# Performance work log

Hardware: AMD Instinct MI355X
Metric: run time of the kernel (lower is better)

The kernel has to match this reference:

```python
import jax, jax.numpy as jnp
import numpy as np

NUM_FRAMES = 6
HEADS = 16
DIM_HEAD = 64


def setup_inputs() -> dict:
    key = jax.random.key(0)
    ks = jax.random.split(key, 7)
    D = 1024
    x = jax.random.normal(ks[0], (12, 1024, D), dtype=jnp.float32)
    context = jax.random.normal(ks[1], (2, 1024, D), dtype=jnp.float32)
    s = 1.0 / np.sqrt(D)
    Wq = jax.random.normal(ks[2], (D, D), dtype=jnp.float32) * s
    Wk = jax.random.normal(ks[3], (D, D), dtype=jnp.float32) * s
    Wv = jax.random.normal(ks[4], (D, D), dtype=jnp.float32) * s
    Wo = jax.random.normal(ks[5], (D, D), dtype=jnp.float32) * s
    bo = jnp.zeros((D,), dtype=jnp.float32)
    return {"x": x, "context": context, "Wq": Wq, "Wk": Wk, "Wv": Wv, "Wo": Wo, "bo": bo}


def reference(x, context, Wq, Wk, Wv, Wo, bo):
    B, S, D = x.shape  # B=12, S=1024, D=1024
    scale = DIM_HEAD ** (-0.5)
    ab = B // NUM_FRAMES  # actual batch after frame inflation
    xr = x.reshape(ab, NUM_FRAMES * S, D)  # [ab, 6144, D]
    # Linear projections (torch Linear: y = x @ W.T)
    q = xr @ Wq.T            # [ab, Sq, inner]
    k = context @ Wk.T       # [ab, Sk, inner]
    v = context @ Wv.T
    Sq = q.shape[1]
    Sk = k.shape[1]
    q = q.reshape(ab, Sq, HEADS, DIM_HEAD).transpose(0, 2, 1, 3)  # [ab,h,Sq,d]
    k = k.reshape(ab, Sk, HEADS, DIM_HEAD).transpose(0, 2, 1, 3)
    v = v.reshape(ab, Sk, HEADS, DIM_HEAD).transpose(0, 2, 1, 3)
    attn = jnp.einsum("bhqd,bhkd->bhqk", q, k) * scale
    attn = jax.nn.softmax(attn, axis=-1)
    out = jnp.einsum("bhqk,bhkd->bhqd", attn, v)
    out = out.transpose(0, 2, 1, 3).reshape(ab, Sq, HEADS * DIM_HEAD)
    out = out @ Wo.T + bo  # dropout is identity at p=0 / eval
    return out.reshape(B, S, D)
```

## Files before the change

kernel.cpp:

```cpp
#include <hip/hip_runtime.h>

typedef short bf16x8 __attribute__((ext_vector_type(8)));
typedef float floatx4 __attribute__((ext_vector_type(4)));
typedef unsigned short u16;
typedef unsigned int u32;

__device__ __forceinline__ u16 f2bf(float f) {
  u32 u = __float_as_uint(f);
  u += 0x7FFF + ((u >> 16) & 1);
  return (u16)(u >> 16);
}
__device__ __forceinline__ u32 packbf(float a, float b) {
  return (u32)f2bf(a) | ((u32)f2bf(b) << 16);
}
__device__ __forceinline__ u32 permpack(u32 a_bits, u32 b_bits) {
  return __builtin_amdgcn_perm(b_bits, a_bits, 0x07060302u);
}

__device__ __forceinline__ float ex2(float x) {
#if __has_builtin(__builtin_amdgcn_exp2f)
  return __builtin_amdgcn_exp2f(x);
#else
  float r;
  asm("v_exp_f32 %0, %1" : "=v"(r) : "v"(x));
  return r;
#endif
}

__device__ __forceinline__ void gload_lds16(const u16* g, u16* l) {
  __builtin_amdgcn_global_load_lds(
      (const __attribute__((address_space(1))) void*)(const void*)g,
      (__attribute__((address_space(3))) void*)(void*)l, 16, 0, 0);
}

__device__ __forceinline__ void bb_mainloop(const u16* __restrict__ A,
                                            const u16* __restrict__ W,
                                            u16* As, u16* Ws, int m0, int n0,
                                            floatx4 acc[4][4]) {
  const int tid = threadIdx.x, lane = tid & 63, w = tid >> 6;
  const int wm = w & 1, wn = w >> 1;
  const int m16 = lane & 15, quad = lane >> 4;
  const int lr = lane >> 2;
  const int sc = (lane & 3) * 8;

  const u16* Ag = A + (size_t)(m0 + w * 32 + lr) * 1024 + sc;
  const u16* Wg = W + (size_t)(n0 + w * 32 + lr) * 1024 + sc;
  u16* const Asl = &As[(w * 32) * 32];
  u16* const Wsl = &Ws[(w * 32) * 32];

#pragma unroll
  for (int i = 0; i < 4; ++i)
#pragma unroll
    for (int j = 0; j < 4; ++j) acc[i][j] = (floatx4)0.0f;

  for (int kt = 0; kt < 32; ++kt) {
    gload_lds16(Ag, Asl);
    gload_lds16(Ag + 16 * 1024, Asl + 16 * 32);
    gload_lds16(Wg, Wsl);
    gload_lds16(Wg + 16 * 1024, Wsl + 16 * 32);
    Ag += 32;
    Wg += 32;
    __syncthreads();
    bf16x8 af[4], bfr[4];
#pragma unroll
    for (int t = 0; t < 4; ++t) {
      af[t]  = *(const bf16x8*)&As[(wm * 64 + t * 16 + m16) * 32 + quad * 8];
      bfr[t] = *(const bf16x8*)&Ws[(wn * 64 + t * 16 + m16) * 32 + quad * 8];
    }
#pragma unroll
    for (int i = 0; i < 4; ++i)
#pragma unroll
      for (int j = 0; j < 4; ++j)
        acc[i][j] = __builtin_amdgcn_mfma_f32_16x16x32_bf16(af[i], bfr[j],
                                                            acc[i][j], 0, 0, 0);
    __syncthreads();
  }
}

__global__ __launch_bounds__(256) void gemm_qkv(
    const u16* __restrict__ xb, const u16* __restrict__ ctxb,
    const u16* __restrict__ wqb, const u16* __restrict__ wkb,
    const u16* __restrict__ wvb, u16* __restrict__ Qb, u16* __restrict__ Kbuf,
    u16* __restrict__ Vtb) {
  __shared__ u16 As[128 * 32];
  __shared__ u16 Ws[128 * 32];
  const int lane = threadIdx.x & 63, w = threadIdx.x >> 6;
  const int wm = w & 1, wn = w >> 1;
  const int m16 = lane & 15, quad = lane >> 4;
  const int y = blockIdx.y;
  const u16 *A, *W;
  int m0, mode;
  if (y < 96)       { A = xb;   W = wqb; m0 = y * 128;         mode = 0; }
  else if (y < 112) { A = ctxb; W = wkb; m0 = (y - 96) * 128;  mode = 1; }
  else              { A = ctxb; W = wvb; m0 = (y - 112) * 128; mode = 2; }
  const int n0 = blockIdx.x * 128;
  floatx4 acc[4][4];
  bb_mainloop(A, W, As, Ws, m0, n0, acc);
  const float cs = (mode == 0) ? 0.18033688011112042f : 1.0f;
#pragma unroll
  for (int j = 0; j < 4; ++j) {
    const int col = n0 + wn * 64 + j * 16 + m16;
#pragma unroll
    for (int i = 0; i < 4; ++i)
#pragma unroll
      for (int r = 0; r < 4; ++r) {
        const int row = m0 + wm * 64 + i * 16 + quad * 4 + r;
        const u16 v = f2bf(acc[i][j][r] * cs);
        if (mode == 0)
          Qb[(size_t)row * 1024 + col] = v;
        else if (mode == 1)
          Kbuf[(size_t)row * 1024 + col] = v;
        else
          Vtb[((size_t)((row >> 10) * 1024 + col)) * 1024 + (row & 1023)] = v;
      }
  }
}

__global__ __launch_bounds__(256) void gemm_out(const u16* __restrict__ A,
                                                const u16* __restrict__ W,
                                                float* __restrict__ C,
                                                const float* __restrict__ bias) {
  __shared__ u16 As[128 * 32];
  __shared__ u16 Ws[128 * 32];
  const int lane = threadIdx.x & 63, w = threadIdx.x >> 6;
  const int wm = w & 1, wn = w >> 1;
  const int m16 = lane & 15, quad = lane >> 4;
  const int n0 = blockIdx.x * 128, m0 = blockIdx.y * 128;
  floatx4 acc[4][4];
  bb_mainloop(A, W, As, Ws, m0, n0, acc);
#pragma unroll
  for (int j = 0; j < 4; ++j) {
    const int col = n0 + wn * 64 + j * 16 + m16;
    const float bv = bias[col];
#pragma unroll
    for (int i = 0; i < 4; ++i)
#pragma unroll
      for (int r = 0; r < 4; ++r) {
        const int row = m0 + wm * 64 + i * 16 + quad * 4 + r;
        C[(size_t)row * 1024 + col] = acc[i][j][r] + bv;
      }
  }
}

__global__ __launch_bounds__(256) void cvt_all(
    const float* __restrict__ x, const float* __restrict__ ctx,
    const float* __restrict__ wq, const float* __restrict__ wk,
    const float* __restrict__ wv, const float* __restrict__ wo,
    u16* __restrict__ xb, u16* __restrict__ ctxb, u16* __restrict__ wqb,
    u16* __restrict__ wkb, u16* __restrict__ wvb, u16* __restrict__ wob) {
  const u32 i = blockIdx.x * 256 + threadIdx.x;
  const float* s;
  u16* d;
  u32 o;
  if (i < 3145728u)      { s = x;   d = xb;   o = i; }
  else if (i < 3670016u) { s = ctx; d = ctxb; o = i - 3145728u; }
  else if (i < 3932160u) { s = wq;  d = wqb;  o = i - 3670016u; }
  else if (i < 4194304u) { s = wk;  d = wkb;  o = i - 3932160u; }
  else if (i < 4456448u) { s = wv;  d = wvb;  o = i - 4194304u; }
  else                   { s = wo;  d = wob;  o = i - 4456448u; }
  const float4 v = ((const float4*)s)[o];
  uint2 p;
  p.x = packbf(v.x, v.y);
  p.y = packbf(v.z, v.w);
  ((uint2*)d)[o] = p;
}

__global__ __launch_bounds__(256, 4) void attn_flash(
    const u16* __restrict__ Q, const u16* __restrict__ Kb,
    const u16* __restrict__ Vt, u16* __restrict__ O) {
  __shared__ u16 Kl[2 * 64 * 32];
  __shared__ u16 Vl[2 * 64 * 32];
  __shared__ u32 Pl[4 * 32 * 36];
  const int tid = threadIdx.x, lane = tid & 63, w = tid >> 6;
  const int m16 = lane & 15, quad = lane >> 4;
  const int h = blockIdx.y, b = blockIdx.z;
  const int q0 = blockIdx.x * 128 + w * 32;
  u32* const pbase = &Pl[w * 32 * 36];

  bf16x8 aq[2][2];
#pragma unroll
  for (int qt = 0; qt < 2; ++qt)
#pragma unroll
    for (int ks = 0; ks < 2; ++ks)
      aq[qt][ks] =
          *(const bf16x8*)&Q[((size_t)(b * 6144 + q0 + qt * 16 + m16)) * 1024 +
                             h * 64 + ks * 32 + quad * 8];

  const int wk = w & 1, wh = w >> 1;
  const u16* kg = Kb + ((size_t)(b * 1024 + wh * 32 + (lane >> 2))) * 1024 +
                  h * 64 + wk * 32 + (lane & 3) * 8;
  const u16* vg = Vt + ((size_t)(b * 16 + h)) * 65536 +
                  (size_t)(wh * 32 + (lane >> 2)) * 1024 + wk * 32 +
                  (lane & 3) * 8;
  u16* const klb = &Kl[wk * 2048 + wh * 1024];
  u16* const vlb = &Vl[wk * 2048 + wh * 1024];

  bf16x8 vone;
#pragma unroll
  for (int e = 0; e < 8; ++e) vone[e] = (short)0x3F80;

  floatx4 oacc[2][4];
#pragma unroll
  for (int qt = 0; qt < 2; ++qt)
#pragma unroll
    for (int mtd = 0; mtd < 4; ++mtd) oacc[qt][mtd] = (floatx4)0.0f;
  floatx4 lacc[2];
  lacc[0] = (floatx4)0.0f;
  lacc[1] = (floatx4)0.0f;

#pragma unroll 1
  for (int kt = 0; kt < 16; ++kt) {
    gload_lds16(kg, klb);
    gload_lds16(kg + 16 * 1024, klb + 512);
    gload_lds16(vg, vlb);
    gload_lds16(vg + 16 * 1024, vlb + 512);
    kg += 64 * 1024;
    vg += 64;
    __syncthreads();

    floatx4 sst[2][4];
#pragma unroll
    for (int mt = 0; mt < 4; ++mt) {
      const int row = mt * 16 + m16;
      const bf16x8 kf0 = *(const bf16x8*)&Kl[row * 32 + quad * 8];
      const bf16x8 kf1 = *(const bf16x8*)&Kl[2048 + row * 32 + quad * 8];
#pragma unroll
      for (int qt = 0; qt < 2; ++qt) {
        floatx4 t = (floatx4)0.0f;
        t = __builtin_amdgcn_mfma_f32_16x16x32_bf16(kf0, aq[qt][0], t, 0, 0, 0);
        sst[qt][mt] =
            __builtin_amdgcn_mfma_f32_16x16x32_bf16(kf1, aq[qt][1], t, 0, 0, 0);
      }
    }
#pragma unroll
    for (int qt = 0; qt < 2; ++qt) {
      u32* const prow = &pbase[(qt * 16 + m16) * 36 + quad * 2];
#pragma unroll
      for (int mt = 0; mt < 4; ++mt) {
        const u32 b0 = __float_as_uint(ex2(sst[qt][mt][0]));
        const u32 b1 = __float_as_uint(ex2(sst[qt][mt][1]));
        const u32 b2 = __float_as_uint(ex2(sst[qt][mt][2]));
        const u32 b3 = __float_as_uint(ex2(sst[qt][mt][3]));
        uint2 pk;
        pk.x = permpack(b0, b1);
        pk.y = permpack(b2, b3);
        *(uint2*)&prow[mt * 8] = pk;
      }
    }
#pragma unroll
    for (int kk = 0; kk < 2; ++kk) {
      bf16x8 pf[2];
#pragma unroll
      for (int qt = 0; qt < 2; ++qt)
        pf[qt] =
            *(const bf16x8*)&pbase[(qt * 16 + m16) * 36 + kk * 16 + quad * 4];
      lacc[0] = __builtin_amdgcn_mfma_f32_16x16x32_bf16(vone, pf[0], lacc[0],
                                                        0, 0, 0);
      lacc[1] = __builtin_amdgcn_mfma_f32_16x16x32_bf16(vone, pf[1], lacc[1],
                                                        0, 0, 0);
#pragma unroll
      for (int mtd = 0; mtd < 4; ++mtd) {
        const bf16x8 vf =
            *(const bf16x8*)&Vl[kk * 2048 + (mtd * 16 + m16) * 32 + quad * 8];
#pragma unroll
        for (int qt = 0; qt < 2; ++qt)
          oacc[qt][mtd] = __builtin_amdgcn_mfma_f32_16x16x32_bf16(
              vf, pf[qt], oacc[qt][mtd], 0, 0, 0);
      }
    }
    __syncthreads();
  }

#pragma unroll
  for (int qt = 0; qt < 2; ++qt) {
    const float linv = 1.0f / lacc[qt][0];
    const size_t obase =
        ((size_t)(b * 6144 + q0 + qt * 16 + m16)) * 1024 + h * 64;
#pragma unroll
    for (int mtd = 0; mtd < 4; ++mtd) {
      const int d0 = mtd * 16 + quad * 4;
      *(u32*)&O[obase + d0] =
          packbf(oacc[qt][mtd][0] * linv, oacc[qt][mtd][1] * linv);
      *(u32*)&O[obase + d0 + 2] =
          packbf(oacc[qt][mtd][2] * linv, oacc[qt][mtd][3] * linv);
    }
  }
}

template <bool A_BF16, bool OUT_F32, int VT, bool BIAS>
__global__ __launch_bounds__(256) void gemm_nt(
    const void* __restrict__ Ap, const float* __restrict__ W,
    void* __restrict__ Cp, const float* __restrict__ bias, int M, int N,
    int K, float scale) {
  __shared__ u16 As[128 * 40];
  __shared__ u16 Ws[128 * 40];
  const int tid = threadIdx.x;
  const int lane = tid & 63;
  const int wv = tid >> 6;
  const int wm = wv & 1, wn = wv >> 1;
  const int m16 = lane & 15, quad = lane >> 4;
  const int n0 = blockIdx.x * 128;
  const int m0 = blockIdx.y * 128;
  const int lr = tid >> 2;
  const int lc = (tid & 3) * 8;
  floatx4 acc[4][4];
#pragma unroll
  for (int i = 0; i < 4; ++i)
#pragma unroll
    for (int j = 0; j < 4; ++j) acc[i][j] = (floatx4)0.0f;
  const int KT = K >> 5;
  for (int kt = 0; kt < KT; ++kt) {
    const int k0 = kt << 5;
#pragma unroll
    for (int j = 0; j < 2; ++j) {
      const int r = lr + 64 * j;
      if (A_BF16) {
        *(uint4*)&As[r * 40 + lc] =
            *(const uint4*)&((const u16*)Ap)[(size_t)(m0 + r) * K + k0 + lc];
      } else {
        const float* Arow = (const float*)Ap + (size_t)(m0 + r) * K + k0 + lc;
        const float4 a0 = *(const float4*)Arow;
        const float4 a1 = *(const float4*)(Arow + 4);
        uint4 p;
        p.x = packbf(a0.x, a0.y); p.y = packbf(a0.z, a0.w);
        p.z = packbf(a1.x, a1.y); p.w = packbf(a1.z, a1.w);
        *(uint4*)&As[r * 40 + lc] = p;
      }
      const float* Wrow = W + (size_t)(n0 + r) * K + k0 + lc;
      const float4 w0 = *(const float4*)Wrow;
      const float4 w1 = *(const float4*)(Wrow + 4);
      uint4 q;
      q.x = packbf(w0.x, w0.y); q.y = packbf(w0.z, w0.w);
      q.z = packbf(w1.x, w1.y); q.w = packbf(w1.z, w1.w);
      *(uint4*)&Ws[r * 40 + lc] = q;
    }
    __syncthreads();
    bf16x8 af[4], bfr[4];
#pragma unroll
    for (int t = 0; t < 4; ++t) {
      af[t]  = *(const bf16x8*)&As[(wm * 64 + t * 16 + m16) * 40 + quad * 8];
      bfr[t] = *(const bf16x8*)&Ws[(wn * 64 + t * 16 + m16) * 40 + quad * 8];
    }
#pragma unroll
    for (int i = 0; i < 4; ++i)
#pragma unroll
      for (int j = 0; j < 4; ++j)
        acc[i][j] = __builtin_amdgcn_mfma_f32_16x16x32_bf16(af[i], bfr[j],
                                                            acc[i][j], 0, 0, 0);
    __syncthreads();
  }
#pragma unroll
  for (int j = 0; j < 4; ++j) {
    const int col = n0 + wn * 64 + j * 16 + m16;
    const float bv = BIAS ? bias[col] : 0.0f;
#pragma unroll
    for (int i = 0; i < 4; ++i)
#pragma unroll
      for (int r = 0; r < 4; ++r) {
        const int row = m0 + wm * 64 + i * 16 + quad * 4 + r;
        const float v = acc[i][j][r] * scale + bv;
        if (OUT_F32)
          ((float*)Cp)[(size_t)row * N + col] = v;
        else if (VT)
          ((u16*)Cp)[((size_t)((row >> 10) * 1024 + col)) * 1024 +
                     (row & 1023)] = f2bf(v);
        else
          ((u16*)Cp)[(size_t)row * N + col] = f2bf(v);
      }
  }
}

extern "C" void kernel_launch(void* const* d_in, const int* in_sizes, int n_in,
                              void* d_out, int out_size, void* d_ws,
                              size_t ws_size, hipStream_t stream) {
  const float* x   = (const float*)d_in[0];
  const float* ctx = (const float*)d_in[1];
  const float* Wq  = (const float*)d_in[2];
  const float* Wk  = (const float*)d_in[3];
  const float* Wv  = (const float*)d_in[4];
  const float* Wo  = (const float*)d_in[5];
  const float* bo  = (const float*)d_in[6];
  float* out = (float*)d_out;
  const dim3 blk(256);
  const float CS = 0.18033688011112042f;

  u16* Qb   = (u16*)d_ws;
  u16* Kbuf = Qb + 12582912;
  u16* Vtb  = Kbuf + 2097152;
  u16* Obx  = Vtb + 2097152;
  u16* ctxb = Obx + 12582912;
  u16* wqb  = ctxb + 2097152;
  u16* wkb  = wqb + 1048576;
  u16* wvb  = wkb + 1048576;
  u16* wob  = wvb + 1048576;
  const size_t need = (size_t)(wob + 1048576 - Qb) * sizeof(u16);

  if (ws_size >= need) {
    cvt_all<<<18432, blk, 0, stream>>>(x, ctx, Wq, Wk, Wv, Wo, Obx, ctxb, wqb,
                                       wkb, wvb, wob);
    gemm_qkv<<<dim3(8, 128), blk, 0, stream>>>(Obx, ctxb, wqb, wkb, wvb, Qb,
                                               Kbuf, Vtb);
    attn_flash<<<dim3(48, 16, 2), blk, 0, stream>>>(Qb, Kbuf, Vtb, Obx);
    gemm_out<<<dim3(8, 96), blk, 0, stream>>>(Obx, wob, out, bo);
  } else {
    gemm_nt<false, false, 0, false><<<dim3(8, 96), blk, 0, stream>>>(
        x, Wq, Qb, nullptr, 12288, 1024, 1024, CS);
    gemm_nt<false, false, 0, false><<<dim3(8, 16), blk, 0, stream>>>(
        ctx, Wk, Kbuf, nullptr, 2048, 1024, 1024, 1.0f);
    gemm_nt<false, false, 1, false><<<dim3(8, 16), blk, 0, stream>>>(
        ctx, Wv, Vtb, nullptr, 2048, 1024, 1024, 1.0f);
    attn_flash<<<dim3(48, 16, 2), blk, 0, stream>>>(Qb, Kbuf, Vtb, Obx);
    gemm_nt<true, true, 0, true><<<dim3(8, 96), blk, 0, stream>>>(
        Obx, Wo, out, bo, 12288, 1024, 1024, 1.0f);
  }
}
```

Baseline: 295.7 us.

## Double-buffer LDS tiles in projection GEMM mainloop to overlap loads with MFMA

```diff
diff --git a/kernel.cpp b/kernel.cpp
--- a/kernel.cpp
+++ b/kernel.cpp
@@ -33,9 +33,35 @@
       (__attribute__((address_space(3))) void*)(void*)l, 16, 0, 0);
 }
 
+__device__ __forceinline__ void bb_stage(const u16* Ag, const u16* Wg,
+                                         u16* Asl, u16* Wsl) {
+  gload_lds16(Ag, Asl);
+  gload_lds16(Ag + 16 * 1024, Asl + 512);
+  gload_lds16(Wg, Wsl);
+  gload_lds16(Wg + 16 * 1024, Wsl + 512);
+}
+
+__device__ __forceinline__ void bb_compute(const u16* As, const u16* Ws,
+                                           int wm, int wn, int m16, int quad,
+                                           floatx4 acc[4][4]) {
+  bf16x8 af[4], bfr[4];
+#pragma unroll
+  for (int t = 0; t < 4; ++t) {
+    af[t]  = *(const bf16x8*)&As[(wm * 64 + t * 16 + m16) * 32 + quad * 8];
+    bfr[t] = *(const bf16x8*)&Ws[(wn * 64 + t * 16 + m16) * 32 + quad * 8];
+  }
+#pragma unroll
+  for (int i = 0; i < 4; ++i)
+#pragma unroll
+    for (int j = 0; j < 4; ++j)
+      acc[i][j] = __builtin_amdgcn_mfma_f32_16x16x32_bf16(af[i], bfr[j],
+                                                          acc[i][j], 0, 0, 0);
+}
+
 __device__ __forceinline__ void bb_mainloop(const u16* __restrict__ A,
                                             const u16* __restrict__ W,
-                                            u16* As, u16* Ws, int m0, int n0,
+                                            u16* As0, u16* Ws0, u16* As1,
+                                            u16* Ws1, int m0, int n0,
                                             floatx4 acc[4][4]) {
   const int tid = threadIdx.x, lane = tid & 63, w = tid >> 6;
   const int wm = w & 1, wn = w >> 1;
@@ -45,34 +71,23 @@
 
   const u16* Ag = A + (size_t)(m0 + w * 32 + lr) * 1024 + sc;
   const u16* Wg = W + (size_t)(n0 + w * 32 + lr) * 1024 + sc;
-  u16* const Asl = &As[(w * 32) * 32];
-  u16* const Wsl = &Ws[(w * 32) * 32];
+  const int so = (w * 32) * 32;
 
 #pragma unroll
   for (int i = 0; i < 4; ++i)
 #pragma unroll
     for (int j = 0; j < 4; ++j) acc[i][j] = (floatx4)0.0f;
 
-  for (int kt = 0; kt < 32; ++kt) {
-    gload_lds16(Ag, Asl);
-    gload_lds16(Ag + 16 * 1024, Asl + 16 * 32);
-    gload_lds16(Wg, Wsl);
-    gload_lds16(Wg + 16 * 1024, Wsl + 16 * 32);
-    Ag += 32;
-    Wg += 32;
-    __syncthreads();
-    bf16x8 af[4], bfr[4];
-#pragma unroll
-    for (int t = 0; t < 4; ++t) {
-      af[t]  = *(const bf16x8*)&As[(wm * 64 + t * 16 + m16) * 32 + quad * 8];
-      bfr[t] = *(const bf16x8*)&Ws[(wn * 64 + t * 16 + m16) * 32 + quad * 8];
-    }
-#pragma unroll
-    for (int i = 0; i < 4; ++i)
-#pragma unroll
-      for (int j = 0; j < 4; ++j)
-        acc[i][j] = __builtin_amdgcn_mfma_f32_16x16x32_bf16(af[i], bfr[j],
-                                                            acc[i][j], 0, 0, 0);
+  bb_stage(Ag, Wg, As0 + so, Ws0 + so);
+  __syncthreads();
+
+  for (int kt = 0; kt < 32; kt += 2) {
+    bb_stage(Ag + (kt + 1) * 32, Wg + (kt + 1) * 32, As1 + so, Ws1 + so);
+    bb_compute(As0, Ws0, wm, wn, m16, quad, acc);
+    __syncthreads();
+    if (kt + 2 < 32)
+      bb_stage(Ag + (kt + 2) * 32, Wg + (kt + 2) * 32, As0 + so, Ws0 + so);
+    bb_compute(As1, Ws1, wm, wn, m16, quad, acc);
     __syncthreads();
   }
 }
@@ -82,8 +97,10 @@
     const u16* __restrict__ wqb, const u16* __restrict__ wkb,
     const u16* __restrict__ wvb, u16* __restrict__ Qb, u16* __restrict__ Kbuf,
     u16* __restrict__ Vtb) {
-  __shared__ u16 As[128 * 32];
-  __shared__ u16 Ws[128 * 32];
+  __shared__ u16 As0[128 * 32];
+  __shared__ u16 Ws0[128 * 32];
+  __shared__ u16 As1[128 * 32];
+  __shared__ u16 Ws1[128 * 32];
   const int lane = threadIdx.x & 63, w = threadIdx.x >> 6;
   const int wm = w & 1, wn = w >> 1;
   const int m16 = lane & 15, quad = lane >> 4;
@@ -95,7 +112,7 @@
   else              { A = ctxb; W = wvb; m0 = (y - 112) * 128; mode = 2; }
   const int n0 = blockIdx.x * 128;
   floatx4 acc[4][4];
-  bb_mainloop(A, W, As, Ws, m0, n0, acc);
+  bb_mainloop(A, W, As0, Ws0, As1, Ws1, m0, n0, acc);
   const float cs = (mode == 0) ? 0.18033688011112042f : 1.0f;
 #pragma unroll
   for (int j = 0; j < 4; ++j) {
@@ -120,14 +137,16 @@
                                                 const u16* __restrict__ W,
                                                 float* __restrict__ C,
                                                 const float* __restrict__ bias) {
-  __shared__ u16 As[128 * 32];
-  __shared__ u16 Ws[128 * 32];
+  __shared__ u16 As0[128 * 32];
+  __shared__ u16 Ws0[128 * 32];
+  __shared__ u16 As1[128 * 32];
+  __shared__ u16 Ws1[128 * 32];
   const int lane = threadIdx.x & 63, w = threadIdx.x >> 6;
   const int wm = w & 1, wn = w >> 1;
   const int m16 = lane & 15, quad = lane >> 4;
   const int n0 = blockIdx.x * 128, m0 = blockIdx.y * 128;
   floatx4 acc[4][4];
-  bb_mainloop(A, W, As, Ws, m0, n0, acc);
+  bb_mainloop(A, W, As0, Ws0, As1, Ws1, m0, n0, acc);
 #pragma unroll
   for (int j = 0; j < 4; ++j) {
     const int col = n0 + wn * 64 + j * 16 + m16;
```

After: 297.6 us. No clear change (+0.6%).
